# Kernel tuning notes

Hardware: AMD Instinct MI355X
Metric: run time of the kernel (lower is better)

Reference implementation:

```python
import jax, jax.numpy as jnp
import numpy as np

B, S, D, H = 128, 512, 256, 512
N_ASSETS = 50
OUT_DIM = N_ASSETS * (N_ASSETS + 1) // 2  # 1275, lower-triangular Cholesky entries


def setup_inputs() -> dict:
    key = jax.random.key(0)
    k = jax.random.split(key, 6)
    x = jax.random.normal(k[0], (B, S, D), dtype=jnp.float32)
    # Layer 0: fused gate weights [D+H, 4H] in gate order (i, f, g, o);
    # equivalent to four separate nn.Linear(D+H, H) layers concatenated.
    W0 = jax.random.normal(k[1], (D + H, 4 * H), jnp.float32) / np.sqrt(D + H)
    b0 = jnp.zeros((4 * H,), jnp.float32).at[H:2 * H].set(1.0)  # forget bias = 1.0
    # Layer 1: input is h of layer 0 -> [H+H, 4H]
    W1 = jax.random.normal(k[2], (2 * H, 4 * H), jnp.float32) / np.sqrt(2 * H)
    b1 = jnp.zeros((4 * H,), jnp.float32).at[H:2 * H].set(1.0)
    Wp = jax.random.normal(k[3], (H, OUT_DIM), jnp.float32) / np.sqrt(H)
    bp = jnp.zeros((OUT_DIM,), jnp.float32)
    return {"x": x, "W0": W0, "b0": b0, "W1": W1, "b1": b1, "Wp": Wp, "bp": bp}


def _cell(xt, h, c, W, b):
    # combined = cat(x, h); single fused GEMM for the 4 gates
    z = jnp.concatenate([xt, h], axis=1) @ W + b  # [B, 4H]
    i, f, g, o = jnp.split(z, 4, axis=1)
    c_new = jax.nn.sigmoid(f) * c + jax.nn.sigmoid(i) * jnp.tanh(g)
    h_new = jax.nn.sigmoid(o) * jnp.tanh(c_new)
    return h_new, c_new


def reference(x, W0, b0, W1, b1, Wp, bp):
    batch = x.shape[0]
    hdim = W0.shape[1] // 4
    init = tuple(jnp.zeros((batch, hdim), x.dtype) for _ in range(4))  # h0,c0,h1,c1

    def step(carry, xt):
        h0, c0, h1, c1 = carry
        h0, c0 = _cell(xt, h0, c0, W0, b0)
        h1, c1 = _cell(h0, h1, c1, W1, b1)
        return (h0, c0, h1, c1), None

    (h0, c0, h1, c1), _ = jax.lax.scan(step, init, jnp.swapaxes(x, 0, 1))
    # Original stacks all timestep outputs but only projects the last hidden state.
    return h1 @ Wp + bp  # [B, OUT_DIM]
```

## Files before the change

### kernel.cpp

```cpp
#include <hip/hip_runtime.h>
#include <stdint.h>

#define BATCH 128
#define SEQ   512
#define DIN   256
#define HID   512
#define NWG   256
#define TPB   512
#define NSLOT 513
#define OUTD  1275
#define HSLOT (BATCH * HID)

typedef __attribute__((ext_vector_type(8))) short bf16x8;
typedef __attribute__((ext_vector_type(4))) unsigned int uint4v;
typedef __attribute__((ext_vector_type(4))) float f32x4;

static __device__ __forceinline__ unsigned short f2bf(float f) {
  unsigned int u = __builtin_bit_cast(unsigned int, f);
  u += 0x7FFFu + ((u >> 16) & 1u);
  return (unsigned short)(u >> 16);
}
static __device__ __forceinline__ float sigmoidf_fast(float v) {
  float e = __expf(-fabsf(v));
  float s = 1.0f / (1.0f + e);
  return v >= 0.0f ? s : 1.0f - s;
}
static __device__ __forceinline__ float tanhf_fast(float v) {
  float e = __expf(-2.0f * fabsf(v));
  float t = (1.0f - e) / (1.0f + e);
  return v >= 0.0f ? t : -t;
}

static __device__ __forceinline__ void ldg_nc(bf16x8& d, const unsigned short* p) {
  asm volatile("global_load_dwordx4 %0, %1, off sc0 sc1" : "=v"(d) : "v"(p));
}
static __device__ __forceinline__ void ldg_nc_dw(unsigned int& d, const unsigned int* p) {
  asm volatile("global_load_dword %0, %1, off sc0 sc1" : "=v"(d) : "v"(p));
}
static __device__ __forceinline__ void stg_nc16(unsigned short* p, uint4v v) {
  asm volatile("global_store_dwordx4 %0, %1, off sc0 sc1" :: "v"(p), "v"(v) : "memory");
}
static __device__ __forceinline__ void stg_nc4(unsigned int* p, unsigned int v) {
  asm volatile("global_store_dword %0, %1, off sc0 sc1" :: "v"(p), "v"(v) : "memory");
}
#define WAIT_TIE1(v) asm volatile("s_waitcnt vmcnt(0)" : "+v"(v) :: "memory")
#define WAIT_TIE4(A)                                                          \
  asm volatile("s_waitcnt vmcnt(0)"                                           \
               : "+v"((A)[0]), "+v"((A)[1]), "+v"((A)[2]), "+v"((A)[3])       \
               :: "memory")
#define WAIT_TIE6(A)                                                          \
  asm volatile("s_waitcnt vmcnt(0)"                                           \
               : "+v"((A)[0]), "+v"((A)[1]), "+v"((A)[2]), "+v"((A)[3]),      \
                 "+v"((A)[4]), "+v"((A)[5]) :: "memory")
#define WAIT_TIE8(A)                                                          \
  asm volatile("s_waitcnt vmcnt(0)"                                           \
               : "+v"((A)[0]), "+v"((A)[1]), "+v"((A)[2]), "+v"((A)[3]),      \
                 "+v"((A)[4]), "+v"((A)[5]), "+v"((A)[6]), "+v"((A)[7])       \
               :: "memory")

__global__ __launch_bounds__(256) void xprep(const float* __restrict__ x,
                                             unsigned short* __restrict__ xb) {
  int p = blockIdx.x;
  int lane = threadIdx.x & 63;
  int g4 = threadIdx.x >> 6;
  int c15 = lane & 15, q = lane >> 4;
  for (int g = 0; g < 16; ++g) {
    int idx = g * 4 + g4;
    int mi = idx >> 3, kt = idx & 7;
    int row = mi * 16 + c15;
    const float* src = x + ((size_t)row * SEQ + p) * DIN + kt * 32 + q * 8;
    f32x4 a = *(const f32x4*)src;
    f32x4 b = *(const f32x4*)(src + 4);
    bf16x8 v;
    v[0] = (short)f2bf(a[0]); v[1] = (short)f2bf(a[1]);
    v[2] = (short)f2bf(a[2]); v[3] = (short)f2bf(a[3]);
    v[4] = (short)f2bf(b[0]); v[5] = (short)f2bf(b[1]);
    v[6] = (short)f2bf(b[2]); v[7] = (short)f2bf(b[3]);
    *(bf16x8*)&xb[((((size_t)p * 8 + mi) * 8 + kt) * 64 + lane) * 8] = v;
  }
}

template <bool USE_XB>
__global__ __launch_bounds__(TPB, 1) void lstm_persistent(
    const float* __restrict__ x, const unsigned short* __restrict__ xb,
    const float* __restrict__ W0, const float* __restrict__ b0,
    const float* __restrict__ W1, const float* __restrict__ b1,
    unsigned int* __restrict__ flags, unsigned short* __restrict__ h0buf,
    unsigned short* __restrict__ h1buf, float* __restrict__ h1fin)
{
  __shared__ unsigned short sWf[4 * 32 * 64 * 8];
  __shared__ float red[4 * 32 * 33];
  __shared__ unsigned short stage[32 * 16];

  const int tid  = threadIdx.x;
  const int wgid = blockIdx.x;
  const int g    = wgid >> 6;
  const int r    = wgid & 63;
  const bool isA = (r < 32);
  const int unit0 = (isA ? r : r - 32) << 4;
  const int lane = tid & 63;
  const int wv   = tid >> 6;
  const int m    = wv & 1;
  const int kq   = wv >> 1;
  const int c15  = lane & 15;
  const int q    = lane >> 4;
  const int miG  = g * 2 + m;
  const int KT   = isA ? 24 : 32;

  {
    const float* W = isA ? W0 : W1;
    for (int f = tid; f < 4 * KT * 64; f += TPB) {
      int ct = f / (KT * 64);
      int rem = f - ct * (KT * 64);
      int kt = rem >> 6, ln = rem & 63;
      int qq = ln >> 4, cc = ln & 15;
      int u_local = ct * 4 + (cc >> 2);
      int gate = cc & 3;
      int gcol = gate * HID + unit0 + u_local;
      int kbase = kt * 32 + qq * 8;
      bf16x8 v;
#pragma unroll
      for (int j = 0; j < 8; ++j)
        v[j] = (short)f2bf(W[(size_t)(kbase + j) * 2048 + gcol]);
      *(bf16x8*)&sWf[(size_t)f * 8] = v;
    }
  }

  const int grow_ = tid >> 3, gu = tid & 7;
  float bias_c[2][4];
  float cst[2] = {0.f, 0.f};
  if (tid < 256) {
    const float* bv = isA ? b0 : b1;
#pragma unroll
    for (int ch = 0; ch < 2; ++ch)
#pragma unroll
      for (int gt = 0; gt < 4; ++gt)
        bias_c[ch][gt] = bv[gt * HID + unit0 + ch * 8 + gu];
  }
  __syncthreads();

  unsigned int* myflags = flags + g * 64;

#define BFRAG(ct, kt) (*(const bf16x8*)&sWf[((((ct) * KT + (kt)) << 6) + lane) << 3])

  for (int p = 0; p < NSLOT; ++p) {
    const unsigned short* h0rd = h0buf + ((p + 1) & 1) * HSLOT;
    unsigned short* h0wr       = h0buf + (p & 1) * HSLOT;
    const unsigned short* h1rd = h1buf + (p & 1) * HSLOT;
    unsigned short* h1wr       = h1buf + ((p + 1) & 1) * HSLOT;
    const bool active = isA ? (p < SEQ) : (p >= 1);

    f32x4 acc[4];
#pragma unroll
    for (int ct = 0; ct < 4; ++ct) acc[ct] = (f32x4){0.f, 0.f, 0.f, 0.f};

    if (isA && active) {
      int ktlo = kq * 6, kthi = ktlo + 6;
      for (int kt = ktlo; kt < kthi && kt < 8; ++kt) {
        bf16x8 ax;
        if (USE_XB) {
          ax = *(const bf16x8*)&xb[((((size_t)p * 8 + miG) * 8 + kt) * 64 + lane) * 8];
        } else {
          const float* xp0 = x + (((size_t)(miG * 16 + c15)) * SEQ + p) * DIN + kt * 32 + q * 8;
          f32x4 a = *(const f32x4*)xp0;
          f32x4 b = *(const f32x4*)(xp0 + 4);
          ax[0] = (short)f2bf(a[0]); ax[1] = (short)f2bf(a[1]);
          ax[2] = (short)f2bf(a[2]); ax[3] = (short)f2bf(a[3]);
          ax[4] = (short)f2bf(b[0]); ax[5] = (short)f2bf(b[1]);
          ax[6] = (short)f2bf(b[2]); ax[7] = (short)f2bf(b[3]);
        }
#pragma unroll
        for (int ct = 0; ct < 4; ++ct)
          acc[ct] = __builtin_amdgcn_mfma_f32_16x16x32_bf16(ax, BFRAG(ct, kt), acc[ct], 0, 0, 0);
      }
    }

    if (wv == 0 && p > 0) {
      const unsigned int* fp = myflags + lane;
      for (;;) {
        unsigned int v;
        ldg_nc_dw(v, fp);
        WAIT_TIE1(v);
        if (__ballot(v >= (unsigned int)p) == ~0ull) break;
        __builtin_amdgcn_s_sleep(1);
      }
    }
    __syncthreads();

    if (active) {
      if (isA) {
        if (kq == 1) {
          bf16x8 ah[4];
#pragma unroll
          for (int i = 0; i < 4; ++i)
            ldg_nc(ah[i], h0rd + ((size_t)(miG * 16 + i) * 64 + lane) * 8);
          WAIT_TIE4(ah);
#pragma unroll
          for (int i = 0; i < 4; ++i)
#pragma unroll
            for (int ct = 0; ct < 4; ++ct)
              acc[ct] = __builtin_amdgcn_mfma_f32_16x16x32_bf16(ah[i], BFRAG(ct, 8 + i), acc[ct], 0, 0, 0);
        } else if (kq >= 2) {
          bf16x8 ah[6];
          int kt0 = kq * 6;
#pragma unroll
          for (int i = 0; i < 6; ++i)
            ldg_nc(ah[i], h0rd + ((size_t)(miG * 16 + (kt0 - 8 + i)) * 64 + lane) * 8);
          WAIT_TIE6(ah);
#pragma unroll
          for (int i = 0; i < 6; ++i)
#pragma unroll
            for (int ct = 0; ct < 4; ++ct)
              acc[ct] = __builtin_amdgcn_mfma_f32_16x16x32_bf16(ah[i], BFRAG(ct, kt0 + i), acc[ct], 0, 0, 0);
        }
      } else {
        bf16x8 ah[8];
        const unsigned short* src = (kq < 2) ? h0rd : h1rd;
        int ktf0 = (kq < 2) ? kq * 8 : (kq - 2) * 8;
#pragma unroll
        for (int i = 0; i < 8; ++i)
          ldg_nc(ah[i], src + ((size_t)(miG * 16 + ktf0 + i) * 64 + lane) * 8);
        WAIT_TIE8(ah);
#pragma unroll
        for (int i = 0; i < 8; ++i)
#pragma unroll
          for (int ct = 0; ct < 4; ++ct)
            acc[ct] = __builtin_amdgcn_mfma_f32_16x16x32_bf16(ah[i], BFRAG(ct, kq * 8 + i), acc[ct], 0, 0, 0);
      }
    }

#pragma unroll
    for (int ch = 0; ch < 2; ++ch) {
      __syncthreads();
      if (active) {
        int lrow = m * 16 + q * 4;
#pragma unroll
        for (int t = 0; t < 2; ++t)
#pragma unroll
          for (int rr = 0; rr < 4; ++rr)
            red[(kq * 32 + lrow + rr) * 33 + t * 16 + c15] = acc[ch * 2 + t][rr];
      }
      __syncthreads();
      if (active && tid < 256) {
        float z[4];
#pragma unroll
        for (int gt = 0; gt < 4; ++gt) {
          float s = bias_c[ch][gt];
          int cidx = gu * 4 + gt;
#pragma unroll
          for (int k2 = 0; k2 < 4; ++k2)
            s += red[(k2 * 32 + grow_) * 33 + cidx];
          z[gt] = s;
        }
        float cn = sigmoidf_fast(z[1]) * cst[ch] + sigmoidf_fast(z[0]) * tanhf_fast(z[2]);
        cst[ch] = cn;
        float hn = sigmoidf_fast(z[3]) * tanhf_fast(cn);
        stage[grow_ * 16 + ch * 8 + gu] = f2bf(hn);
        if (!isA && p == NSLOT - 1)
          h1fin[(size_t)(g * 32 + grow_) * HID + unit0 + ch * 8 + gu] = hn;
      }
    }
    __syncthreads();

    if (wv == 0) {
      if (active && tid < 64) {
        int row = tid >> 1, qq2 = tid & 1;
        uint4v v = *(const uint4v*)&stage[row * 16 + qq2 * 8];
        int mi = g * 2 + (row >> 4), r15 = row & 15;
        int ktu = unit0 >> 5;
        int qu = ((unit0 & 31) >> 3) + qq2;
        unsigned short* dst = (isA ? h0wr : h1wr) +
            ((size_t)(mi * 16 + ktu) * 64 + qu * 16 + r15) * 8;
        stg_nc16(dst, v);
      }
      asm volatile("s_waitcnt vmcnt(0)" ::: "memory");
      if (tid == 0) stg_nc4(myflags + r, (unsigned int)(p + 1));
    }
  }
#undef BFRAG
}

__global__ __launch_bounds__(256) void proj_kernel(
    const float* __restrict__ h1, const float* __restrict__ Wp,
    const float* __restrict__ bp, float* __restrict__ out)
{
  int o = blockIdx.x * 256 + threadIdx.x;
  int b = blockIdx.y;
  if (o >= OUTD) return;
  const float* hr = h1 + (size_t)b * HID;
  float acc = bp[o];
#pragma unroll 8
  for (int k = 0; k < HID; ++k)
    acc = fmaf(hr[k], Wp[(size_t)k * OUTD + o], acc);
  out[(size_t)b * OUTD + o] = acc;
}

extern "C" void kernel_launch(void* const* d_in, const int* in_sizes, int n_in,
                              void* d_out, int out_size, void* d_ws, size_t ws_size,
                              hipStream_t stream) {
  const float* x  = (const float*)d_in[0];
  const float* W0 = (const float*)d_in[1];
  const float* b0 = (const float*)d_in[2];
  const float* W1 = (const float*)d_in[3];
  const float* b1 = (const float*)d_in[4];
  const float* Wp = (const float*)d_in[5];
  const float* bp = (const float*)d_in[6];
  float* out = (float*)d_out;

  char* ws = (char*)d_ws;
  unsigned int* flags = (unsigned int*)ws;
  unsigned short* h0b = (unsigned short*)(ws + 4096);
  unsigned short* h1b = (unsigned short*)(ws + 4096 + 262144);
  float* h1fin        = (float*)(ws + 4096 + 2 * 262144);
  unsigned short* xbp = (unsigned short*)(ws + 4096 + 3 * 262144);
  const size_t need_xb = 4096 + 3 * 262144 + (size_t)SEQ * BATCH * DIN * 2;
  const bool use_xb = (ws_size >= need_xb);

  hipMemsetAsync(d_ws, 0, 4096 + 2 * 262144, stream);
  if (use_xb) {
    hipLaunchKernelGGL(xprep, dim3(SEQ), dim3(256), 0, stream, x, xbp);
    hipLaunchKernelGGL(lstm_persistent<true>, dim3(NWG), dim3(TPB), 0, stream,
                       x, xbp, W0, b0, W1, b1, flags, h0b, h1b, h1fin);
  } else {
    hipLaunchKernelGGL(lstm_persistent<false>, dim3(NWG), dim3(TPB), 0, stream,
                       x, xbp, W0, b0, W1, b1, flags, h0b, h1b, h1fin);
  }
  hipLaunchKernelGGL(proj_kernel, dim3((OUTD + 255) / 256, BATCH), dim3(256), 0, stream,
                     h1fin, Wp, bp, out);
}
```

Before: 2.630 ms.

## Split batch rows into two pipelined halves with atomic counter barriers

```diff
diff --git a/kernel.cpp b/kernel.cpp
--- a/kernel.cpp
+++ b/kernel.cpp
@@ -6,7 +6,7 @@
 #define DIN   256
 #define HID   512
 #define NWG   256
-#define TPB   512
+#define TPB   256
 #define NSLOT 513
 #define OUTD  1275
 #define HSLOT (BATCH * HID)
@@ -39,9 +39,6 @@
 }
 static __device__ __forceinline__ void stg_nc16(unsigned short* p, uint4v v) {
   asm volatile("global_store_dwordx4 %0, %1, off sc0 sc1" :: "v"(p), "v"(v) : "memory");
-}
-static __device__ __forceinline__ void stg_nc4(unsigned int* p, unsigned int v) {
-  asm volatile("global_store_dword %0, %1, off sc0 sc1" :: "v"(p), "v"(v) : "memory");
 }
 #define WAIT_TIE1(v) asm volatile("s_waitcnt vmcnt(0)" : "+v"(v) :: "memory")
 #define WAIT_TIE4(A)                                                          \
@@ -85,27 +82,26 @@
     const float* __restrict__ x, const unsigned short* __restrict__ xb,
     const float* __restrict__ W0, const float* __restrict__ b0,
     const float* __restrict__ W1, const float* __restrict__ b1,
-    unsigned int* __restrict__ flags, unsigned short* __restrict__ h0buf,
+    unsigned int* __restrict__ cnts, unsigned short* __restrict__ h0buf,
     unsigned short* __restrict__ h1buf, float* __restrict__ h1fin)
 {
   __shared__ unsigned short sWf[4 * 32 * 64 * 8];
-  __shared__ float red[4 * 32 * 33];
-  __shared__ unsigned short stage[32 * 16];
+  __shared__ float red[4 * 16 * 66];
+  __shared__ unsigned short stg2[2][16 * 16];
 
   const int tid  = threadIdx.x;
   const int wgid = blockIdx.x;
-  const int g    = wgid >> 6;
+  const int set  = wgid >> 6;
   const int r    = wgid & 63;
   const bool isA = (r < 32);
   const int unit0 = (isA ? r : r - 32) << 4;
   const int lane = tid & 63;
-  const int wv   = tid >> 6;
-  const int m    = wv & 1;
-  const int kq   = wv >> 1;
+  const int kq   = tid >> 6;
   const int c15  = lane & 15;
   const int q    = lane >> 4;
-  const int miG  = g * 2 + m;
   const int KT   = isA ? 24 : 32;
+  const int ktu  = unit0 >> 5;
+  const int qbase = (unit0 >> 3) & 3;
 
   {
     const float* W = isA ? W0 : W1;
@@ -114,9 +110,7 @@
       int rem = f - ct * (KT * 64);
       int kt = rem >> 6, ln = rem & 63;
       int qq = ln >> 4, cc = ln & 15;
-      int u_local = ct * 4 + (cc >> 2);
-      int gate = cc & 3;
-      int gcol = gate * HID + unit0 + u_local;
+      int gcol = (cc & 3) * HID + unit0 + ct * 4 + (cc >> 2);
       int kbase = kt * 32 + qq * 8;
       bf16x8 v;
 #pragma unroll
@@ -126,20 +120,18 @@
     }
   }
 
-  const int grow_ = tid >> 3, gu = tid & 7;
-  float bias_c[2][4];
+  const int grow = tid >> 4, gu = tid & 15;
+  float bias_g[4];
+  {
+    const float* bv = isA ? b0 : b1;
+#pragma unroll
+    for (int gt = 0; gt < 4; ++gt)
+      bias_g[gt] = bv[gt * HID + unit0 + gu];
+  }
   float cst[2] = {0.f, 0.f};
-  if (tid < 256) {
-    const float* bv = isA ? b0 : b1;
-#pragma unroll
-    for (int ch = 0; ch < 2; ++ch)
-#pragma unroll
-      for (int gt = 0; gt < 4; ++gt)
-        bias_c[ch][gt] = bv[gt * HID + unit0 + ch * 8 + gu];
-  }
   __syncthreads();
 
-  unsigned int* myflags = flags + g * 64;
+  unsigned int* cntH[2] = {cnts + (set * 2 + 0) * 32, cnts + (set * 2 + 1) * 32};
 
 #define BFRAG(ct, kt) (*(const bf16x8*)&sWf[((((ct) * KT + (kt)) << 6) + lane) << 3])
 
@@ -149,132 +141,132 @@
     const unsigned short* h1rd = h1buf + (p & 1) * HSLOT;
     unsigned short* h1wr       = h1buf + ((p + 1) & 1) * HSLOT;
     const bool active = isA ? (p < SEQ) : (p >= 1);
-
-    f32x4 acc[4];
-#pragma unroll
-    for (int ct = 0; ct < 4; ++ct) acc[ct] = (f32x4){0.f, 0.f, 0.f, 0.f};
-
-    if (isA && active) {
-      int ktlo = kq * 6, kthi = ktlo + 6;
-      for (int kt = ktlo; kt < kthi && kt < 8; ++kt) {
-        bf16x8 ax;
-        if (USE_XB) {
-          ax = *(const bf16x8*)&xb[((((size_t)p * 8 + miG) * 8 + kt) * 64 + lane) * 8];
+    const unsigned int target = (unsigned int)(64 * p);
+
+#pragma unroll
+    for (int half = 0; half < 2; ++half) {
+      const int miG = set * 2 + half;
+
+      f32x4 acc[4];
+#pragma unroll
+      for (int ct = 0; ct < 4; ++ct) acc[ct] = (f32x4){0.f, 0.f, 0.f, 0.f};
+
+      if (isA && active) {
+        int ktlo = kq * 6, kthi = ktlo + 6;
+        for (int kt = ktlo; kt < kthi && kt < 8; ++kt) {
+          bf16x8 ax;
+          if (USE_XB) {
+            ax = *(const bf16x8*)&xb[((((size_t)p * 8 + miG) * 8 + kt) * 64 + lane) * 8];
+          } else {
+            const float* xp0 = x + (((size_t)(miG * 16 + c15)) * SEQ + p) * DIN + kt * 32 + q * 8;
+            f32x4 a = *(const f32x4*)xp0;
+            f32x4 b = *(const f32x4*)(xp0 + 4);
+            ax[0] = (short)f2bf(a[0]); ax[1] = (short)f2bf(a[1]);
+            ax[2] = (short)f2bf(a[2]); ax[3] = (short)f2bf(a[3]);
+            ax[4] = (short)f2bf(b[0]); ax[5] = (short)f2bf(b[1]);
+            ax[6] = (short)f2bf(b[2]); ax[7] = (short)f2bf(b[3]);
+          }
+#pragma unroll
+          for (int ct = 0; ct < 4; ++ct)
+            acc[ct] = __builtin_amdgcn_mfma_f32_16x16x32_bf16(ax, BFRAG(ct, kt), acc[ct], 0, 0, 0);
+        }
+      }
+
+      if (tid == 0 && p > 0) {
+        const unsigned int* cp = cntH[half];
+        for (;;) {
+          unsigned int v;
+          ldg_nc_dw(v, cp);
+          WAIT_TIE1(v);
+          if (v >= target) break;
+          __builtin_amdgcn_s_sleep(1);
+        }
+      }
+      __syncthreads();
+
+      if (active) {
+        if (isA) {
+          if (kq == 1) {
+            bf16x8 ah[4];
+#pragma unroll
+            for (int i = 0; i < 4; ++i)
+              ldg_nc(ah[i], h0rd + ((size_t)(miG * 16 + i) * 64 + lane) * 8);
+            WAIT_TIE4(ah);
+#pragma unroll
+            for (int i = 0; i < 4; ++i)
+#pragma unroll
+              for (int ct = 0; ct < 4; ++ct)
+                acc[ct] = __builtin_amdgcn_mfma_f32_16x16x32_bf16(ah[i], BFRAG(ct, 8 + i), acc[ct], 0, 0, 0);
+          } else if (kq >= 2) {
+            bf16x8 ah[6];
+            int kt0 = kq * 6;
+#pragma unroll
+            for (int i = 0; i < 6; ++i)
+              ldg_nc(ah[i], h0rd + ((size_t)(miG * 16 + (kt0 - 8 + i)) * 64 + lane) * 8);
+            WAIT_TIE6(ah);
+#pragma unroll
+            for (int i = 0; i < 6; ++i)
+#pragma unroll
+              for (int ct = 0; ct < 4; ++ct)
+                acc[ct] = __builtin_amdgcn_mfma_f32_16x16x32_bf16(ah[i], BFRAG(ct, kt0 + i), acc[ct], 0, 0, 0);
+          }
         } else {
-          const float* xp0 = x + (((size_t)(miG * 16 + c15)) * SEQ + p) * DIN + kt * 32 + q * 8;
-          f32x4 a = *(const f32x4*)xp0;
-          f32x4 b = *(const f32x4*)(xp0 + 4);
-          ax[0] = (short)f2bf(a[0]); ax[1] = (short)f2bf(a[1]);
-          ax[2] = (short)f2bf(a[2]); ax[3] = (short)f2bf(a[3]);
-          ax[4] = (short)f2bf(b[0]); ax[5] = (short)f2bf(b[1]);
-          ax[6] = (short)f2bf(b[2]); ax[7] = (short)f2bf(b[3]);
-        }
+          bf16x8 ah[8];
+          const unsigned short* src = (kq < 2) ? h0rd : h1rd;
+          int ktf0 = (kq < 2) ? kq * 8 : (kq - 2) * 8;
+#pragma unroll
+          for (int i = 0; i < 8; ++i)
+            ldg_nc(ah[i], src + ((size_t)(miG * 16 + ktf0 + i) * 64 + lane) * 8);
+          WAIT_TIE8(ah);
+#pragma unroll
+          for (int i = 0; i < 8; ++i)
+#pragma unroll
+            for (int ct = 0; ct < 4; ++ct)
+              acc[ct] = __builtin_amdgcn_mfma_f32_16x16x32_bf16(ah[i], BFRAG(ct, kq * 8 + i), acc[ct], 0, 0, 0);
+        }
+      }
+
+      if (active) {
 #pragma unroll
         for (int ct = 0; ct < 4; ++ct)
-          acc[ct] = __builtin_amdgcn_mfma_f32_16x16x32_bf16(ax, BFRAG(ct, kt), acc[ct], 0, 0, 0);
-      }
-    }
-
-    if (wv == 0 && p > 0) {
-      const unsigned int* fp = myflags + lane;
-      for (;;) {
-        unsigned int v;
-        ldg_nc_dw(v, fp);
-        WAIT_TIE1(v);
-        if (__ballot(v >= (unsigned int)p) == ~0ull) break;
-        __builtin_amdgcn_s_sleep(1);
-      }
-    }
-    __syncthreads();
-
-    if (active) {
-      if (isA) {
-        if (kq == 1) {
-          bf16x8 ah[4];
-#pragma unroll
-          for (int i = 0; i < 4; ++i)
-            ldg_nc(ah[i], h0rd + ((size_t)(miG * 16 + i) * 64 + lane) * 8);
-          WAIT_TIE4(ah);
-#pragma unroll
-          for (int i = 0; i < 4; ++i)
-#pragma unroll
-            for (int ct = 0; ct < 4; ++ct)
-              acc[ct] = __builtin_amdgcn_mfma_f32_16x16x32_bf16(ah[i], BFRAG(ct, 8 + i), acc[ct], 0, 0, 0);
-        } else if (kq >= 2) {
-          bf16x8 ah[6];
-          int kt0 = kq * 6;
-#pragma unroll
-          for (int i = 0; i < 6; ++i)
-            ldg_nc(ah[i], h0rd + ((size_t)(miG * 16 + (kt0 - 8 + i)) * 64 + lane) * 8);
-          WAIT_TIE6(ah);
-#pragma unroll
-          for (int i = 0; i < 6; ++i)
-#pragma unroll
-            for (int ct = 0; ct < 4; ++ct)
-              acc[ct] = __builtin_amdgcn_mfma_f32_16x16x32_bf16(ah[i], BFRAG(ct, kt0 + i), acc[ct], 0, 0, 0);
-        }
-      } else {
-        bf16x8 ah[8];
-        const unsigned short* src = (kq < 2) ? h0rd : h1rd;
-        int ktf0 = (kq < 2) ? kq * 8 : (kq - 2) * 8;
-#pragma unroll
-        for (int i = 0; i < 8; ++i)
-          ldg_nc(ah[i], src + ((size_t)(miG * 16 + ktf0 + i) * 64 + lane) * 8);
-        WAIT_TIE8(ah);
-#pragma unroll
-        for (int i = 0; i < 8; ++i)
-#pragma unroll
-          for (int ct = 0; ct < 4; ++ct)
-            acc[ct] = __builtin_amdgcn_mfma_f32_16x16x32_bf16(ah[i], BFRAG(ct, kq * 8 + i), acc[ct], 0, 0, 0);
-      }
-    }
-
-#pragma unroll
-    for (int ch = 0; ch < 2; ++ch) {
+#pragma unroll
+          for (int rr = 0; rr < 4; ++rr)
+            red[(kq * 16 + q * 4 + rr) * 66 + ct * 16 + c15] = acc[ct][rr];
+      }
       __syncthreads();
+
       if (active) {
-        int lrow = m * 16 + q * 4;
-#pragma unroll
-        for (int t = 0; t < 2; ++t)
-#pragma unroll
-          for (int rr = 0; rr < 4; ++rr)
-            red[(kq * 32 + lrow + rr) * 33 + t * 16 + c15] = acc[ch * 2 + t][rr];
+        float z[4];
+#pragma unroll
+        for (int gt = 0; gt < 4; ++gt) {
+          float s = bias_g[gt];
+#pragma unroll
+          for (int k2 = 0; k2 < 4; ++k2)
+            s += red[(k2 * 16 + grow) * 66 + gu * 4 + gt];
+          z[gt] = s;
+        }
+        float cn = sigmoidf_fast(z[1]) * cst[half] + sigmoidf_fast(z[0]) * tanhf_fast(z[2]);
+        cst[half] = cn;
+        float hn = sigmoidf_fast(z[3]) * tanhf_fast(cn);
+        stg2[half][grow * 16 + gu] = f2bf(hn);
+        if (!isA && p == NSLOT - 1)
+          h1fin[(size_t)(set * 32 + half * 16 + grow) * HID + unit0 + gu] = hn;
       }
       __syncthreads();
-      if (active && tid < 256) {
-        float z[4];
-#pragma unroll
-        for (int gt = 0; gt < 4; ++gt) {
-          float s = bias_c[ch][gt];
-          int cidx = gu * 4 + gt;
-#pragma unroll
-          for (int k2 = 0; k2 < 4; ++k2)
-            s += red[(k2 * 32 + grow_) * 33 + cidx];
-          z[gt] = s;
-        }
-        float cn = sigmoidf_fast(z[1]) * cst[ch] + sigmoidf_fast(z[0]) * tanhf_fast(z[2]);
-        cst[ch] = cn;
-        float hn = sigmoidf_fast(z[3]) * tanhf_fast(cn);
-        stage[grow_ * 16 + ch * 8 + gu] = f2bf(hn);
-        if (!isA && p == NSLOT - 1)
-          h1fin[(size_t)(g * 32 + grow_) * HID + unit0 + ch * 8 + gu] = hn;
-      }
-    }
-    __syncthreads();
-
-    if (wv == 0) {
-      if (active && tid < 64) {
-        int row = tid >> 1, qq2 = tid & 1;
-        uint4v v = *(const uint4v*)&stage[row * 16 + qq2 * 8];
-        int mi = g * 2 + (row >> 4), r15 = row & 15;
-        int ktu = unit0 >> 5;
-        int qu = ((unit0 & 31) >> 3) + qq2;
-        unsigned short* dst = (isA ? h0wr : h1wr) +
-            ((size_t)(mi * 16 + ktu) * 64 + qu * 16 + r15) * 8;
-        stg_nc16(dst, v);
-      }
-      asm volatile("s_waitcnt vmcnt(0)" ::: "memory");
-      if (tid == 0) stg_nc4(myflags + r, (unsigned int)(p + 1));
+
+      if (kq == 0) {
+        if (active && lane < 32) {
+          int row = lane >> 1, qq2 = lane & 1;
+          uint4v v = *(const uint4v*)&stg2[half][row * 16 + qq2 * 8];
+          unsigned short* dst = (isA ? h0wr : h1wr) +
+              ((size_t)(miG * 16 + ktu) * 64 + (qbase + qq2) * 16 + row) * 8;
+          stg_nc16(dst, v);
+        }
+        asm volatile("s_waitcnt vmcnt(0)" ::: "memory");
+        if (tid == 0)
+          (void)__hip_atomic_fetch_add(cntH[half], 1u, __ATOMIC_RELAXED,
+                                       __HIP_MEMORY_SCOPE_AGENT);
+      }
     }
   }
 #undef BFRAG
@@ -308,7 +300,7 @@
   float* out = (float*)d_out;
 
   char* ws = (char*)d_ws;
-  unsigned int* flags = (unsigned int*)ws;
+  unsigned int* cnts  = (unsigned int*)ws;
   unsigned short* h0b = (unsigned short*)(ws + 4096);
   unsigned short* h1b = (unsigned short*)(ws + 4096 + 262144);
   float* h1fin        = (float*)(ws + 4096 + 2 * 262144);
@@ -320,10 +312,10 @@
   if (use_xb) {
     hipLaunchKernelGGL(xprep, dim3(SEQ), dim3(256), 0, stream, x, xbp);
     hipLaunchKernelGGL(lstm_persistent<true>, dim3(NWG), dim3(TPB), 0, stream,
-                       x, xbp, W0, b0, W1, b1, flags, h0b, h1b, h1fin);
+                       x, xbp, W0, b0, W1, b1, cnts, h0b, h1b, h1fin);
   } else {
     hipLaunchKernelGGL(lstm_persistent<false>, dim3(NWG), dim3(TPB), 0, stream,
-                       x, xbp, W0, b0, W1, b1, flags, h0b, h1b, h1fin);
+                       x, xbp, W0, b0, W1, b1, cnts, h0b, h1b, h1fin);
   }
   hipLaunchKernelGGL(proj_kernel, dim3((OUTD + 255) / 256, BATCH), dim3(256), 0, stream,
                      h1fin, Wp, bp, out);
```

Measured after the change: 4.315 ms. 64.1% more time.
